# Performance work log

Hardware: AMD Instinct MI355X
Metric: run time of the kernel (lower is better)

## Reference

```python
import jax, jax.numpy as jnp
import numpy as np

EPS = 1e-5
N, DEG, D, L = 50000, 16, 128, 2  # nodes, max_neighbor, embed_size, gnn_layer


def _log_map_zero(y):
    # Poincare ball log map at origin: atanh(||y||) * y / ||y||, with clamps
    n = jnp.linalg.norm(y, axis=-1, keepdims=True)
    nc = jnp.clip(n, EPS, 1.0 - EPS)
    return y * (jnp.arctanh(nc) / nc)


def _exp_map_zero(v):
    # Poincare ball exp map at origin: tanh(||v||) * v / ||v||
    n = jnp.linalg.norm(v, axis=-1, keepdims=True)
    nc = jnp.maximum(n, EPS)
    return v * (jnp.tanh(nc) / nc)


def setup_inputs() -> dict:
    key = jax.random.key(0)
    k1, k2, k3, k4, k5 = jax.random.split(key, 5)
    node_repr = jax.random.normal(k1, (N, D), jnp.float32) * 0.1
    adj = jax.random.randint(k2, (N, DEG), 0, N)
    weight = jax.random.normal(k3, (N, DEG), jnp.float32)
    mask = jnp.ones((N, 1), jnp.float32)
    # per-relation, per-layer message weights (2 relations: pos / neg edges)
    scale = 1.0 / np.sqrt(D)
    W_pos = jax.random.normal(k4, (L, D, D), jnp.float32) * scale
    W_neg = jax.random.normal(k5, (L, D, D), jnp.float32) * scale
    return {"node_repr": node_repr, "adj": adj, "weight": weight,
            "mask": mask, "W_pos": W_pos, "W_neg": W_neg}


def reference(node_repr, adj, weight, mask, W_pos, W_neg):
    # split_graph_by_negative_edge
    pos_m = (weight > 0).astype(weight.dtype)
    neg_m = (weight < 0).astype(weight.dtype)
    adjs = (adj * pos_m.astype(adj.dtype), adj * neg_m.astype(adj.dtype))
    ws = (weight * pos_m, (-weight) * neg_m)
    Ws = (W_pos, W_neg)

    x = node_repr
    for step in range(L):
        x = (_log_map_zero(x) if step > 0 else x) * mask
        combined = jnp.zeros_like(x)
        for a, w, W in zip(adjs, ws, Ws):
            msg = (x @ W[step]) * mask                    # [N, D]
            nb = msg[a.reshape(-1)].reshape(N, DEG, D)    # neighbor gather
            combined = combined + jnp.sum(w[..., None] * nb, axis=1)
        combined = combined * mask                        # dropout identity (eval)
        x = _exp_map_zero(combined) * mask
        x = jax.nn.relu(x) * mask                         # poincare activation
    return x
```

## Files before the change

kernel.cpp:

```cpp
#include <hip/hip_runtime.h>
#include <math.h>

#define DD 128
#define DEG 16
#define TMG 16
#define TMZ 32
#define LDST 136
#define EPSV 1e-5f

typedef _Float16 half8_t __attribute__((ext_vector_type(8)));
typedef float    f32x4   __attribute__((ext_vector_type(4)));
typedef signed char c16v __attribute__((ext_vector_type(16)));

__device__ __forceinline__ float fast_tanh_over(float n) {
    float e  = __expf(2.f * n);
    float th = 1.f - __fdividef(2.f, e + 1.f);
    return __fdividef(th, n);
}
__device__ __forceinline__ float fast_atanh_over(float n) {
    float r = 0.5f * __logf(__fdividef(1.f + n, 1.f - n));
    return __fdividef(r, n);
}

__global__ void prepW(const float* __restrict__ Wp, const float* __restrict__ Wn,
                      _Float16* __restrict__ WT)
{
    int bid   = blockIdx.x;
    int mat   = bid >> 3;
    int chunk = bid & 7;
    int l = mat >> 1, rel = mat & 1;
    const float* __restrict__ src = (rel ? Wn : Wp) + (size_t)l * DD * DD;
    _Float16* __restrict__ dst = WT + (size_t)mat * DD * DD;
    for (int o = chunk * 2048 + threadIdx.x; o < chunk * 2048 + 2048; o += 256) {
        int nn = o >> 7, kk = o & 127;
        dst[o] = (_Float16)src[kk * DD + nn];
    }
}

__global__ __launch_bounds__(256, 2) void z_gemm(
    const float* __restrict__ xf32,
    const signed char* __restrict__ y8,
    const float* __restrict__ ysc,
    const float* __restrict__ mask,
    const _Float16* __restrict__ WTp, const _Float16* __restrict__ WTn,
    signed char* __restrict__ Z8,
    float* __restrict__ zscP, float* __restrict__ zscN,
    int n, int layer0)
{
    __shared__ __align__(16) _Float16 At[TMZ][LDST];

    const int row0 = blockIdx.x * TMZ;
    const int tid  = threadIdx.x;

    {
        const int ar   = tid >> 3;
        const int ac   = (tid & 7) * 16;
        const int rowg = row0 + ar;
        _Float16 hv[16];
        if (rowg < n) {
            if (layer0) {
                float m = mask[rowg]; float m2 = m * m;
                const float4* xp = (const float4*)(xf32 + (size_t)rowg * DD + ac);
                #pragma unroll
                for (int q4 = 0; q4 < 4; ++q4) {
                    float4 v = xp[q4];
                    hv[q4*4+0] = (_Float16)(v.x*m2); hv[q4*4+1] = (_Float16)(v.y*m2);
                    hv[q4*4+2] = (_Float16)(v.z*m2); hv[q4*4+3] = (_Float16)(v.w*m2);
                }
            } else {
                float s = ysc[rowg];
                c16v v = *(const c16v*)(y8 + (size_t)rowg * DD + ac);
                #pragma unroll
                for (int c = 0; c < 16; ++c) hv[c] = (_Float16)((float)v[c] * s);
            }
        } else {
            #pragma unroll
            for (int c = 0; c < 16; ++c) hv[c] = (_Float16)0.f;
        }
        *(half8_t*)&At[ar][ac]     = *(half8_t*)&hv[0];
        *(half8_t*)&At[ar][ac + 8] = *(half8_t*)&hv[8];
    }
    __syncthreads();

    const int w    = tid >> 6;
    const int mt   = w >> 1;
    const int rel  = w & 1;
    const int l64  = tid & 63;
    const int l15  = l64 & 15;
    const int quad = l64 >> 4;

    half8_t aF[4];
    #pragma unroll
    for (int kb = 0; kb < 4; ++kb)
        aF[kb] = *(const half8_t*)&At[mt * 16 + l15][kb * 32 + quad * 8];

    const _Float16* __restrict__ WT = rel ? WTn : WTp;
    f32x4 acc[8];
    #pragma unroll
    for (int nb = 0; nb < 8; ++nb) acc[nb] = (f32x4){0.f, 0.f, 0.f, 0.f};
    #pragma unroll
    for (int nb = 0; nb < 8; ++nb) {
        const _Float16* bp = WT + (size_t)(nb * 16 + l15) * DD + quad * 8;
        #pragma unroll
        for (int kb = 0; kb < 4; ++kb)
            acc[nb] = __builtin_amdgcn_mfma_f32_16x16x32_f16(
                aF[kb], *(const half8_t*)(bp + kb * 32), acc[nb], 0, 0, 0);
    }

    signed char* __restrict__ zb  = Z8 + (size_t)rel * n * DD;
    float*       __restrict__ zsc = rel ? zscN : zscP;
    #pragma unroll
    for (int r = 0; r < 4; ++r) {
        const int rowg = row0 + mt * 16 + quad * 4 + r;
        float mx = 0.f;
        #pragma unroll
        for (int nb = 0; nb < 8; ++nb) mx = fmaxf(mx, fabsf(acc[nb][r]));
        mx = fmaxf(mx, __shfl_xor(mx, 1));
        mx = fmaxf(mx, __shfl_xor(mx, 2));
        mx = fmaxf(mx, __shfl_xor(mx, 4));
        mx = fmaxf(mx, __shfl_xor(mx, 8));
        if (rowg < n) {
            float qs = __fdividef(127.f, fmaxf(mx, 1e-20f));
            signed char* zr = zb + (size_t)rowg * DD + l15;
            #pragma unroll
            for (int nb = 0; nb < 8; ++nb)
                zr[nb * 16] = (signed char)__float2int_rn(acc[nb][r] * qs);
            if (l15 == 0) zsc[rowg] = mx * (1.f / 127.f);
        }
    }
}

__global__ __launch_bounds__(256, 2) void gather_ep(
    const signed char* __restrict__ Z8,
    const float* __restrict__ zscP, const float* __restrict__ zscN,
    const int*   __restrict__ adj, const float* __restrict__ wgt,
    const float* __restrict__ mask,
    float* __restrict__ dst_f32,
    signed char* __restrict__ dst8, float* __restrict__ dst_scale,
    int n, int apply_logmap)
{
    __shared__ int   eoffS[TMG][DEG];
    __shared__ float ewgtS[TMG][DEG];
    __shared__ float msh[TMG];

    const int row0 = blockIdx.x * TMG;
    const int tid  = threadIdx.x;

    {
        const int nd = tid >> 4, eg = tid & 15;
        int   av = adj[(size_t)(row0 + nd) * DEG + eg];
        float wv = wgt[(size_t)(row0 + nd) * DEG + eg];
        const int sel = (wv > 0.f) ? 0 : 1;
        const float* sp = sel ? zscN : zscP;
        eoffS[nd][eg] = av * DD + sel * (n * DD);
        ewgtS[nd][eg] = fabsf(wv) * sp[av];
        if (tid < TMG) msh[tid] = mask[row0 + tid];
    }
    __syncthreads();

    const int l64  = tid & 63;
    const int node = (tid >> 6) * 4 + (l64 >> 4);
    const int e    = (l64 >> 3) & 1;
    const int g    = l64 & 7;

    int   offl[8];
    float wl[8];
    #pragma unroll
    for (int j = 0; j < 8; ++j) {
        offl[j] = eoffS[node][2 * j + e];
        wl[j]   = ewgtS[node][2 * j + e];
    }

    float a[16];
    #pragma unroll
    for (int c = 0; c < 16; ++c) a[c] = 0.f;
    const signed char* __restrict__ srcg = Z8 + g * 16;
    #pragma unroll
    for (int j = 0; j < 8; ++j) {
        c16v v = *(const c16v*)(srcg + (size_t)offl[j]);
        float wj = wl[j];
        #pragma unroll
        for (int c = 0; c < 16; ++c) a[c] += wj * (float)v[c];
    }
    float f[8];
    #pragma unroll
    for (int c = 0; c < 8; ++c) {
        float own  = e ? a[8 + c] : a[c];
        float send = e ? a[c]     : a[8 + c];
        f[c] = own + __shfl_xor(send, 8);
    }

    const int   row = row0 + node;
    const float m   = msh[node];
    float t[8];
    float p = 0.f;
    #pragma unroll
    for (int c = 0; c < 8; ++c) { float cv = f[c] * m; t[c] = cv; p += cv * cv; }
    p += __shfl_xor(p, 1); p += __shfl_xor(p, 2);
    p += __shfl_xor(p, 4); p += __shfl_xor(p, 8);
    float nc = fmaxf(sqrtf(p), EPSV);
    float sc = fast_tanh_over(nc);
    float s2 = 0.f;
    #pragma unroll
    for (int c = 0; c < 8; ++c) {
        t[c] = fmaxf(t[c] * sc * m, 0.f) * m;
        s2 += t[c] * t[c];
    }

    if (apply_logmap) {
        s2 += __shfl_xor(s2, 1); s2 += __shfl_xor(s2, 2);
        s2 += __shfl_xor(s2, 4); s2 += __shfl_xor(s2, 8);
        float nc2 = fminf(fmaxf(sqrtf(s2), EPSV), 1.f - EPSV);
        float ff  = fast_atanh_over(nc2) * m * m;
        float y[8], rmax = 0.f;
        #pragma unroll
        for (int c = 0; c < 8; ++c) { y[c] = t[c] * ff; rmax = fmaxf(rmax, fabsf(y[c])); }
        rmax = fmaxf(rmax, __shfl_xor(rmax, 1));
        rmax = fmaxf(rmax, __shfl_xor(rmax, 2));
        rmax = fmaxf(rmax, __shfl_xor(rmax, 4));
        rmax = fmaxf(rmax, __shfl_xor(rmax, 8));
        float qs = __fdividef(127.f, fmaxf(rmax, 1e-20f));
        int q[8];
        #pragma unroll
        for (int c = 0; c < 8; ++c) q[c] = __float2int_rn(y[c] * qs);
        unsigned lo = (q[0]&255) | ((q[1]&255)<<8) | ((q[2]&255)<<16) | ((unsigned)(q[3]&255)<<24);
        unsigned hi = (q[4]&255) | ((q[5]&255)<<8) | ((q[6]&255)<<16) | ((unsigned)(q[7]&255)<<24);
        *(uint2*)(dst8 + (size_t)row * DD + g * 16 + e * 8) = make_uint2(lo, hi);
        if ((l64 & 15) == 0) dst_scale[row] = rmax * (1.f / 127.f);
    } else {
        float* drow = dst_f32 + (size_t)row * DD + g * 16 + e * 8;
        ((float4*)drow)[0] = make_float4(t[0], t[1], t[2], t[3]);
        ((float4*)drow)[1] = make_float4(t[4], t[5], t[6], t[7]);
    }
}

extern "C" void kernel_launch(void* const* d_in, const int* in_sizes, int n_in,
                              void* d_out, int out_size, void* d_ws, size_t ws_size,
                              hipStream_t stream)
{
    const float* node_repr = (const float*)d_in[0];
    const int*   adj       = (const int*)  d_in[1];
    const float* weight    = (const float*)d_in[2];
    const float* mask      = (const float*)d_in[3];
    const float* W_pos     = (const float*)d_in[4];
    const float* W_neg     = (const float*)d_in[5];

    const int n = in_sizes[0] / DD;

    signed char* Z8   = (signed char*)d_ws;
    signed char* y8   = Z8 + (size_t)2 * n * DD;
    float*       zscP = (float*)(y8 + (size_t)n * DD);
    float*       zscN = zscP + n;
    float*       ysc  = zscN + n;
    _Float16*    WT   = (_Float16*)(ysc + n);

    prepW<<<32, 256, 0, stream>>>(W_pos, W_neg, WT);

    dim3 zgrid((n + TMZ - 1) / TMZ);
    dim3 ggrid((n + TMG - 1) / TMG);

    z_gemm<<<zgrid, 256, 0, stream>>>(node_repr, nullptr, nullptr, mask,
                                      WT + 0 * DD * DD, WT + 1 * DD * DD,
                                      Z8, zscP, zscN, n, 1);
    gather_ep<<<ggrid, 256, 0, stream>>>(Z8, zscP, zscN, adj, weight, mask,
                                         nullptr, y8, ysc, n, 1);
    z_gemm<<<zgrid, 256, 0, stream>>>(nullptr, y8, ysc, mask,
                                      WT + 2 * DD * DD, WT + 3 * DD * DD,
                                      Z8, zscP, zscN, n, 0);
    gather_ep<<<ggrid, 256, 0, stream>>>(Z8, zscP, zscN, adj, weight, mask,
                                         (float*)d_out, nullptr, nullptr, n, 0);
}
```

Before: 191.6 us.

## Fuse layer-0 gather epilogue with layer-1 GEMM into one kernel

Merges the first gather/exp-log epilogue with the second layer's message GEMM. The log-mapped activations go to shared memory as fp16 and feed MFMA directly, so the int8 intermediate y8 and its scale are no longer written and read back, and one kernel launch is dropped. Z1 gets its own workspace buffer so the fused kernel never overwrites Z0 while other blocks still read it. In exchange, each 16-row block now runs a small GEMM with its own W loads and extra syncs, which may lower GEMM efficiency compared with the 32-row tiles of the separate GEMM kernel.

```diff
diff --git a/kernel.cpp b/kernel.cpp
--- a/kernel.cpp
+++ b/kernel.cpp
@@ -37,41 +37,29 @@
     }
 }
 
-__global__ __launch_bounds__(256, 2) void z_gemm(
-    const float* __restrict__ xf32,
-    const signed char* __restrict__ y8,
-    const float* __restrict__ ysc,
-    const float* __restrict__ mask,
+__global__ __launch_bounds__(256, 2) void z_gemm0(
+    const float* __restrict__ xf32, const float* __restrict__ mask,
     const _Float16* __restrict__ WTp, const _Float16* __restrict__ WTn,
-    signed char* __restrict__ Z8,
-    float* __restrict__ zscP, float* __restrict__ zscN,
-    int n, int layer0)
+    signed char* __restrict__ Z8, float* __restrict__ zscP,
+    float* __restrict__ zscN, int n)
 {
     __shared__ __align__(16) _Float16 At[TMZ][LDST];
 
     const int row0 = blockIdx.x * TMZ;
     const int tid  = threadIdx.x;
-
     {
         const int ar   = tid >> 3;
         const int ac   = (tid & 7) * 16;
         const int rowg = row0 + ar;
         _Float16 hv[16];
         if (rowg < n) {
-            if (layer0) {
-                float m = mask[rowg]; float m2 = m * m;
-                const float4* xp = (const float4*)(xf32 + (size_t)rowg * DD + ac);
-                #pragma unroll
-                for (int q4 = 0; q4 < 4; ++q4) {
-                    float4 v = xp[q4];
-                    hv[q4*4+0] = (_Float16)(v.x*m2); hv[q4*4+1] = (_Float16)(v.y*m2);
-                    hv[q4*4+2] = (_Float16)(v.z*m2); hv[q4*4+3] = (_Float16)(v.w*m2);
-                }
-            } else {
-                float s = ysc[rowg];
-                c16v v = *(const c16v*)(y8 + (size_t)rowg * DD + ac);
-                #pragma unroll
-                for (int c = 0; c < 16; ++c) hv[c] = (_Float16)((float)v[c] * s);
+            float m = mask[rowg]; float m2 = m * m;
+            const float4* xp = (const float4*)(xf32 + (size_t)rowg * DD + ac);
+            #pragma unroll
+            for (int q4 = 0; q4 < 4; ++q4) {
+                float4 v = xp[q4];
+                hv[q4*4+0] = (_Float16)(v.x*m2); hv[q4*4+1] = (_Float16)(v.y*m2);
+                hv[q4*4+2] = (_Float16)(v.z*m2); hv[q4*4+3] = (_Float16)(v.w*m2);
             }
         } else {
             #pragma unroll
@@ -130,18 +118,20 @@
     }
 }
 
-__global__ __launch_bounds__(256, 2) void gather_ep(
-    const signed char* __restrict__ Z8,
-    const float* __restrict__ zscP, const float* __restrict__ zscN,
+__global__ __launch_bounds__(256, 2) void fused_mid(
+    const signed char* __restrict__ Z0,
+    const float* __restrict__ zsc0P, const float* __restrict__ zsc0N,
     const int*   __restrict__ adj, const float* __restrict__ wgt,
     const float* __restrict__ mask,
-    float* __restrict__ dst_f32,
-    signed char* __restrict__ dst8, float* __restrict__ dst_scale,
-    int n, int apply_logmap)
+    const _Float16* __restrict__ WT1p, const _Float16* __restrict__ WT1n,
+    signed char* __restrict__ Z1,
+    float* __restrict__ zsc1P, float* __restrict__ zsc1N, int n)
 {
     __shared__ int   eoffS[TMG][DEG];
     __shared__ float ewgtS[TMG][DEG];
     __shared__ float msh[TMG];
+    __shared__ __align__(16) _Float16 yt[TMG][LDST];
+    __shared__ float partQ[2][2][TMG];
 
     const int row0 = blockIdx.x * TMG;
     const int tid  = threadIdx.x;
@@ -151,7 +141,7 @@
         int   av = adj[(size_t)(row0 + nd) * DEG + eg];
         float wv = wgt[(size_t)(row0 + nd) * DEG + eg];
         const int sel = (wv > 0.f) ? 0 : 1;
-        const float* sp = sel ? zscN : zscP;
+        const float* sp = sel ? zsc0N : zsc0P;
         eoffS[nd][eg] = av * DD + sel * (n * DD);
         ewgtS[nd][eg] = fabsf(wv) * sp[av];
         if (tid < TMG) msh[tid] = mask[row0 + tid];
@@ -174,7 +164,7 @@
     float a[16];
     #pragma unroll
     for (int c = 0; c < 16; ++c) a[c] = 0.f;
-    const signed char* __restrict__ srcg = Z8 + g * 16;
+    const signed char* __restrict__ srcg = Z0 + g * 16;
     #pragma unroll
     for (int j = 0; j < 8; ++j) {
         c16v v = *(const c16v*)(srcg + (size_t)offl[j]);
@@ -190,8 +180,7 @@
         f[c] = own + __shfl_xor(send, 8);
     }
 
-    const int   row = row0 + node;
-    const float m   = msh[node];
+    const float m = msh[node];
     float t[8];
     float p = 0.f;
     #pragma unroll
@@ -206,32 +195,143 @@
         t[c] = fmaxf(t[c] * sc * m, 0.f) * m;
         s2 += t[c] * t[c];
     }
-
-    if (apply_logmap) {
-        s2 += __shfl_xor(s2, 1); s2 += __shfl_xor(s2, 2);
-        s2 += __shfl_xor(s2, 4); s2 += __shfl_xor(s2, 8);
-        float nc2 = fminf(fmaxf(sqrtf(s2), EPSV), 1.f - EPSV);
-        float ff  = fast_atanh_over(nc2) * m * m;
-        float y[8], rmax = 0.f;
-        #pragma unroll
-        for (int c = 0; c < 8; ++c) { y[c] = t[c] * ff; rmax = fmaxf(rmax, fabsf(y[c])); }
-        rmax = fmaxf(rmax, __shfl_xor(rmax, 1));
-        rmax = fmaxf(rmax, __shfl_xor(rmax, 2));
-        rmax = fmaxf(rmax, __shfl_xor(rmax, 4));
-        rmax = fmaxf(rmax, __shfl_xor(rmax, 8));
+    s2 += __shfl_xor(s2, 1); s2 += __shfl_xor(s2, 2);
+    s2 += __shfl_xor(s2, 4); s2 += __shfl_xor(s2, 8);
+    float nc2 = fminf(fmaxf(sqrtf(s2), EPSV), 1.f - EPSV);
+    float ff  = fast_atanh_over(nc2) * m * m;
+    half8_t hy;
+    #pragma unroll
+    for (int c = 0; c < 8; ++c) hy[c] = (_Float16)(t[c] * ff);
+    *(half8_t*)&yt[node][g * 16 + e * 8] = hy;
+    __syncthreads();
+
+    const int w    = tid >> 6;
+    const int rel  = w >> 1;
+    const int ch   = w & 1;
+    const int l15  = l64 & 15;
+    const int quad = l64 >> 4;
+
+    half8_t aF[4];
+    #pragma unroll
+    for (int kb = 0; kb < 4; ++kb)
+        aF[kb] = *(const half8_t*)&yt[l15][kb * 32 + quad * 8];
+
+    const _Float16* __restrict__ WT = rel ? WT1n : WT1p;
+    f32x4 acc[4];
+    #pragma unroll
+    for (int nb = 0; nb < 4; ++nb) acc[nb] = (f32x4){0.f, 0.f, 0.f, 0.f};
+    #pragma unroll
+    for (int nb = 0; nb < 4; ++nb) {
+        const _Float16* bp = WT + (size_t)((ch * 4 + nb) * 16 + l15) * DD + quad * 8;
+        #pragma unroll
+        for (int kb = 0; kb < 4; ++kb)
+            acc[nb] = __builtin_amdgcn_mfma_f32_16x16x32_f16(
+                aF[kb], *(const half8_t*)(bp + kb * 32), acc[nb], 0, 0, 0);
+    }
+
+    #pragma unroll
+    for (int r = 0; r < 4; ++r) {
+        float mx = 0.f;
+        #pragma unroll
+        for (int nb = 0; nb < 4; ++nb) mx = fmaxf(mx, fabsf(acc[nb][r]));
+        mx = fmaxf(mx, __shfl_xor(mx, 1));
+        mx = fmaxf(mx, __shfl_xor(mx, 2));
+        mx = fmaxf(mx, __shfl_xor(mx, 4));
+        mx = fmaxf(mx, __shfl_xor(mx, 8));
+        if (l15 == 0) partQ[rel][ch][quad * 4 + r] = mx;
+    }
+    __syncthreads();
+
+    signed char* __restrict__ zb  = Z1 + (size_t)rel * n * DD;
+    float*       __restrict__ zsc = rel ? zsc1N : zsc1P;
+    #pragma unroll
+    for (int r = 0; r < 4; ++r) {
+        const int rl   = quad * 4 + r;
+        const int rowg = row0 + rl;
+        float rmax = fmaxf(partQ[rel][0][rl], partQ[rel][1][rl]);
         float qs = __fdividef(127.f, fmaxf(rmax, 1e-20f));
-        int q[8];
-        #pragma unroll
-        for (int c = 0; c < 8; ++c) q[c] = __float2int_rn(y[c] * qs);
-        unsigned lo = (q[0]&255) | ((q[1]&255)<<8) | ((q[2]&255)<<16) | ((unsigned)(q[3]&255)<<24);
-        unsigned hi = (q[4]&255) | ((q[5]&255)<<8) | ((q[6]&255)<<16) | ((unsigned)(q[7]&255)<<24);
-        *(uint2*)(dst8 + (size_t)row * DD + g * 16 + e * 8) = make_uint2(lo, hi);
-        if ((l64 & 15) == 0) dst_scale[row] = rmax * (1.f / 127.f);
-    } else {
-        float* drow = dst_f32 + (size_t)row * DD + g * 16 + e * 8;
-        ((float4*)drow)[0] = make_float4(t[0], t[1], t[2], t[3]);
-        ((float4*)drow)[1] = make_float4(t[4], t[5], t[6], t[7]);
-    }
+        signed char* zr = zb + (size_t)rowg * DD + ch * 64 + l15;
+        #pragma unroll
+        for (int nb = 0; nb < 4; ++nb)
+            zr[nb * 16] = (signed char)__float2int_rn(acc[nb][r] * qs);
+        if (ch == 0 && l15 == 0) zsc[rowg] = rmax * (1.f / 127.f);
+    }
+}
+
+__global__ __launch_bounds__(256, 2) void gather_final(
+    const signed char* __restrict__ Z1,
+    const float* __restrict__ zsc1P, const float* __restrict__ zsc1N,
+    const int*   __restrict__ adj, const float* __restrict__ wgt,
+    const float* __restrict__ mask,
+    float* __restrict__ dst_f32, int n)
+{
+    __shared__ int   eoffS[TMG][DEG];
+    __shared__ float ewgtS[TMG][DEG];
+    __shared__ float msh[TMG];
+
+    const int row0 = blockIdx.x * TMG;
+    const int tid  = threadIdx.x;
+    {
+        const int nd = tid >> 4, eg = tid & 15;
+        int   av = adj[(size_t)(row0 + nd) * DEG + eg];
+        float wv = wgt[(size_t)(row0 + nd) * DEG + eg];
+        const int sel = (wv > 0.f) ? 0 : 1;
+        const float* sp = sel ? zsc1N : zsc1P;
+        eoffS[nd][eg] = av * DD + sel * (n * DD);
+        ewgtS[nd][eg] = fabsf(wv) * sp[av];
+        if (tid < TMG) msh[tid] = mask[row0 + tid];
+    }
+    __syncthreads();
+
+    const int l64  = tid & 63;
+    const int node = (tid >> 6) * 4 + (l64 >> 4);
+    const int e    = (l64 >> 3) & 1;
+    const int g    = l64 & 7;
+
+    int   offl[8];
+    float wl[8];
+    #pragma unroll
+    for (int j = 0; j < 8; ++j) {
+        offl[j] = eoffS[node][2 * j + e];
+        wl[j]   = ewgtS[node][2 * j + e];
+    }
+
+    float a[16];
+    #pragma unroll
+    for (int c = 0; c < 16; ++c) a[c] = 0.f;
+    const signed char* __restrict__ srcg = Z1 + g * 16;
+    #pragma unroll
+    for (int j = 0; j < 8; ++j) {
+        c16v v = *(const c16v*)(srcg + (size_t)offl[j]);
+        float wj = wl[j];
+        #pragma unroll
+        for (int c = 0; c < 16; ++c) a[c] += wj * (float)v[c];
+    }
+    float f[8];
+    #pragma unroll
+    for (int c = 0; c < 8; ++c) {
+        float own  = e ? a[8 + c] : a[c];
+        float send = e ? a[c]     : a[8 + c];
+        f[c] = own + __shfl_xor(send, 8);
+    }
+
+    const int   row = row0 + node;
+    const float m   = msh[node];
+    float t[8];
+    float p = 0.f;
+    #pragma unroll
+    for (int c = 0; c < 8; ++c) { float cv = f[c] * m; t[c] = cv; p += cv * cv; }
+    p += __shfl_xor(p, 1); p += __shfl_xor(p, 2);
+    p += __shfl_xor(p, 4); p += __shfl_xor(p, 8);
+    float nc = fmaxf(sqrtf(p), EPSV);
+    float sc = fast_tanh_over(nc);
+    #pragma unroll
+    for (int c = 0; c < 8; ++c)
+        t[c] = fmaxf(t[c] * sc * m, 0.f) * m;
+
+    float* drow = dst_f32 + (size_t)row * DD + g * 16 + e * 8;
+    ((float4*)drow)[0] = make_float4(t[0], t[1], t[2], t[3]);
+    ((float4*)drow)[1] = make_float4(t[4], t[5], t[6], t[7]);
 }
 
 extern "C" void kernel_launch(void* const* d_in, const int* in_sizes, int n_in,
@@ -247,26 +347,25 @@
 
     const int n = in_sizes[0] / DD;
 
-    signed char* Z8   = (signed char*)d_ws;
-    signed char* y8   = Z8 + (size_t)2 * n * DD;
-    float*       zscP = (float*)(y8 + (size_t)n * DD);
-    float*       zscN = zscP + n;
-    float*       ysc  = zscN + n;
-    _Float16*    WT   = (_Float16*)(ysc + n);
+    signed char* Z0    = (signed char*)d_ws;
+    signed char* Z1    = Z0 + (size_t)2 * n * DD;
+    float*       zsc0P = (float*)(Z1 + (size_t)2 * n * DD);
+    float*       zsc0N = zsc0P + n;
+    float*       zsc1P = zsc0N + n;
+    float*       zsc1N = zsc1P + n;
+    _Float16*    WT    = (_Float16*)(zsc1N + n);
 
     prepW<<<32, 256, 0, stream>>>(W_pos, W_neg, WT);
 
     dim3 zgrid((n + TMZ - 1) / TMZ);
     dim3 ggrid((n + TMG - 1) / TMG);
 
-    z_gemm<<<zgrid, 256, 0, stream>>>(node_repr, nullptr, nullptr, mask,
-                                      WT + 0 * DD * DD, WT + 1 * DD * DD,
-                                      Z8, zscP, zscN, n, 1);
-    gather_ep<<<ggrid, 256, 0, stream>>>(Z8, zscP, zscN, adj, weight, mask,
-                                         nullptr, y8, ysc, n, 1);
-    z_gemm<<<zgrid, 256, 0, stream>>>(nullptr, y8, ysc, mask,
-                                      WT + 2 * DD * DD, WT + 3 * DD * DD,
-                                      Z8, zscP, zscN, n, 0);
-    gather_ep<<<ggrid, 256, 0, stream>>>(Z8, zscP, zscN, adj, weight, mask,
-                                         (float*)d_out, nullptr, nullptr, n, 0);
-}
+    z_gemm0<<<zgrid, 256, 0, stream>>>(node_repr, mask,
+                                       WT + 0 * DD * DD, WT + 1 * DD * DD,
+                                       Z0, zsc0P, zsc0N, n);
+    fused_mid<<<ggrid, 256, 0, stream>>>(Z0, zsc0P, zsc0N, adj, weight, mask,
+                                         WT + 2 * DD * DD, WT + 3 * DD * DD,
+                                         Z1, zsc1P, zsc1N, n);
+    gather_final<<<ggrid, 256, 0, stream>>>(Z1, zsc1P, zsc1N, adj, weight, mask,
+                                            (float*)d_out, n);
+}
```

New measurement: 180.4 us. -5.8%, faster.
